# Kernel optimization log

Measured on AMD Instinct MI355X. Metric: run time of the kernel, lower is better.

## Reference

```python
import jax, jax.numpy as jnp
import numpy as np

# Dimensions (match init_kwargs / input_specs)
B, T, D, H, HH, E, L = 256, 512, 256, 256, 128, 32, 2


def setup_inputs() -> dict:
    key = jax.random.key(0)
    ks = jax.random.split(key, 8)
    f32 = jnp.float32
    s_ih = 1.0 / np.sqrt(D)
    s_hh = 1.0 / np.sqrt(H)
    s_hy = 1.0 / np.sqrt(D + H)
    s_hh_hy = 1.0 / np.sqrt(HH)
    s_z = 1.0 / np.sqrt(HH)
    s_d = 1.0 / np.sqrt(E)
    return {
        "input": jax.random.normal(ks[0], (B, T, D), f32),
        # main-cell weights, stacked over layers (layer1 input = hidden = D)
        "Wih": jax.random.normal(ks[1], (L, H, D), f32) * s_ih,
        "Whh": jax.random.normal(ks[2], (L, H, H), f32) * s_hh,
        "b": jnp.zeros((L, H), f32),
        # hyper (meta) RNN cell: input is concat(x_t, h_{t-1})
        "Wih_hy": jax.random.normal(ks[3], (L, HH, D + H), f32) * s_hy,
        "Whh_hy": jax.random.normal(ks[4], (L, HH, HH), f32) * s_hh_hy,
        "b_hy": jnp.zeros((L, HH), f32),
        # embedding projections: hyper_h -> z for (x-scale, h-scale, bias), then z -> d
        "Whz": jax.random.normal(ks[5], (L, 3, E, HH), f32) * s_z,
        "bz": jnp.ones((L, 3, E), f32),  # init z to 1 so d starts near a plain RNN
        "Wzd": jax.random.normal(ks[6], (L, 3, H, E), f32) * s_d,
    }


def reference(input, Wih, Whh, b, Wih_hy, Whh_hy, b_hy, Whz, bz, Wzd):
    """MetaRNN (HyperNetwork-conditioned RNN): for each layer, a small hyper RNN
    consumes [x_t, h_{t-1}] and emits embeddings z that generate per-unit scales
    d_x, d_h and a dynamic bias d_b for the main tanh RNN cell.
    Returns (all hidden states [B,T,H], last hidden state [B,H])."""
    Bb = input.shape[0]
    dt = input.dtype
    x_seq = input
    for l in range(L):
        # input-to-hidden GEMM for the whole sequence, hoisted out of the scan
        xW = jnp.einsum('btd,hd->bth', x_seq, Wih[l])  # [B,T,H]
        Whh_l, b_l = Whh[l], b[l]
        Wih_hy_l, Whh_hy_l, b_hy_l = Wih_hy[l], Whh_hy[l], b_hy[l]
        Whz_l, bz_l, Wzd_l = Whz[l], bz[l], Wzd[l]

        def step(carry, inp):
            h, hh = carry           # main hidden [B,H], hyper hidden [B,HH]
            x_t, xW_t = inp
            hyp_in = jnp.concatenate([x_t, h], axis=1)          # [B, D+H]
            hh_new = jnp.tanh(hyp_in @ Wih_hy_l.T + hh @ Whh_hy_l.T + b_hy_l)
            z = jnp.einsum('bk,gek->bge', hh_new, Whz_l) + bz_l  # [B,3,E]
            d = jnp.einsum('bge,ghe->bgh', z, Wzd_l)             # [B,3,H]
            h_new = jnp.tanh(d[:, 0] * xW_t + d[:, 1] * (h @ Whh_l.T)
                             + d[:, 2] + b_l)
            return (h_new, hh_new), h_new

        h0 = jnp.zeros((Bb, H), dt)
        hh0 = jnp.zeros((Bb, HH), dt)
        xs = (jnp.swapaxes(x_seq, 0, 1), jnp.swapaxes(xW, 0, 1))  # time-major
        _, ys = jax.lax.scan(step, (h0, hh0), xs)
        x_seq = jnp.swapaxes(ys, 0, 1)  # [B,T,H]
    return (x_seq, x_seq[:, -1, :])
```

## Files before the change

### kernel.cpp

```cpp
#include <hip/hip_runtime.h>


#define DEVI __device__ __forceinline__

typedef __bf16 bf16x8 __attribute__((ext_vector_type(8)));
typedef float f32x4 __attribute__((ext_vector_type(4)));
typedef unsigned short u16;
typedef unsigned int u32;
typedef u32 u32x4 __attribute__((ext_vector_type(4)));
typedef u16 u16x8 __attribute__((ext_vector_type(8)));

constexpr int B_ = 256, T_ = 512, D_ = 256, H_ = 256, HH_ = 128, E_ = 32;
constexpr int BT = B_ * T_;

constexpr int OXW = 0,      PXW = 16 * 8 * 512;
constexpr int OXH = 131072, PXH = 8 * 8 * 512;
constexpr int OHY = 196608, PHY = 8 * 12 * 512;
constexpr int OWHH = 294912, PWHH = 16 * 8 * 512;
constexpr int OWHZ = 425984, PWHZ = 6 * 4 * 512;
constexpr int OWZD = 450560, PWZD = 48 * 512;
constexpr int LSTRIDE = 499712;

constexpr size_t WS_XW = 0;
constexpr size_t WS_XH = (size_t)BT * H_ * 4;
constexpr size_t WS_FR = WS_XH + (size_t)BT * HH_ * 4;

DEVI u16 f2bf(float v) {
  u32 u = __float_as_uint(v);
  u += 0x7fffu + ((u >> 16) & 1u);
  return (u16)(u >> 16);
}
DEVI float bf2f(u16 s) { return __uint_as_float(((u32)s) << 16); }
DEVI void split2(float v, u16 &hi, u16 &lo) {
  hi = f2bf(v);
  lo = f2bf(v - bf2f(hi));
}
DEVI bf16x8 ldfrag(const u16 *p) {
  u32x4 v = *reinterpret_cast<const u32x4 *>(p);
  return __builtin_bit_cast(bf16x8, v);
}
DEVI f32x4 mfma3(bf16x8 ah, bf16x8 al, bf16x8 bh, bf16x8 bl, f32x4 c) {
  c = __builtin_amdgcn_mfma_f32_16x16x32_bf16(ah, bh, c, 0, 0, 0);
  c = __builtin_amdgcn_mfma_f32_16x16x32_bf16(ah, bl, c, 0, 0, 0);
  c = __builtin_amdgcn_mfma_f32_16x16x32_bf16(al, bh, c, 0, 0, 0);
  return c;
}
DEVI float tanh_fast(float x) {
  float e = __expf(2.0f * x);
  return 1.0f - 2.0f / (e + 1.0f);
}
DEVI void block_sync() {
  asm volatile("s_waitcnt lgkmcnt(0)\n\ts_barrier" ::: "memory");
}

__global__ void metarnn_prep(const float *__restrict__ Wih,
                             const float *__restrict__ Whh,
                             const float *__restrict__ Wih_hy,
                             const float *__restrict__ Whh_hy,
                             const float *__restrict__ Whz,
                             const float *__restrict__ Wzd,
                             u16 *__restrict__ fr) {
  int gid = blockIdx.x * 256 + threadIdx.x;
  int lane = gid & 63;
  int e = gid >> 6;
  if (e >= 2 * 488) return;
  int l = e / 488, r = e - l * 488;
  u16 *base = fr + (size_t)l * LSTRIDE;
  int rowL = lane & 15, kg = (lane >> 4) << 3;

  const float *src = nullptr;
  int ld = 0, nt = 0, kt = 0, KT = 1, special = 0;
  u16 *dh = nullptr, *dl = nullptr;
  if (r < 128) {
    nt = r >> 3; kt = r & 7; KT = 8;
    src = Wih + (size_t)l * H_ * D_; ld = D_;
    dh = base + OXW; dl = dh + PXW;
  } else if (r < 192) {
    r -= 128; nt = r >> 3; kt = r & 7; KT = 8;
    src = Wih_hy + (size_t)l * HH_ * (D_ + H_); ld = D_ + H_;
    dh = base + OXH; dl = dh + PXH;
  } else if (r < 288) {
    r -= 192; nt = r / 12; kt = r - nt * 12; KT = 12; special = 1;
    dh = base + OHY; dl = dh + PHY;
  } else if (r < 416) {
    r -= 288; nt = r >> 3; kt = r & 7; KT = 8;
    src = Whh + (size_t)l * H_ * H_; ld = H_;
    dh = base + OWHH; dl = dh + PWHH;
  } else if (r < 440) {
    r -= 416; nt = r >> 2; kt = r & 3; KT = 4;
    src = Whz + (size_t)l * 3 * E_ * HH_; ld = HH_;
    dh = base + OWHZ; dl = dh + PWHZ;
  } else {
    r -= 440; int g = r >> 4; nt = r & 15; kt = 0; KT = 1;
    src = Wzd + (size_t)(l * 3 + g) * H_ * E_; ld = E_;
    dh = base + OWZD + g * 16 * 512; dl = base + OWZD + PWZD + g * 16 * 512;
  }
  int row = nt * 16 + rowL;
  long dof = ((long)(nt * KT + kt) * 64 + lane) * 8;
  for (int j = 0; j < 8; ++j) {
    int k = kt * 32 + kg + j;
    float v;
    if (special) {
      v = (k < 256) ? Wih_hy[((size_t)l * HH_ + row) * (D_ + H_) + 256 + k]
                    : Whh_hy[((size_t)l * HH_ + row) * HH_ + (k - 256)];
    } else {
      v = src[(size_t)row * ld + k];
    }
    u16 hi, lo;
    split2(v, hi, lo);
    dh[dof + j] = hi;
    dl[dof + j] = lo;
  }
}

__global__ __launch_bounds__(256, 1) void metarnn_gemm(
    const float *__restrict__ x, const u16 *__restrict__ fr,
    float *__restrict__ xW, float *__restrict__ xH) {
  int w = threadIdx.x >> 6, lane = threadIdx.x & 63;
  int m0 = blockIdx.x * 32;
  int rowL = lane & 15, kg = (lane >> 4) << 3;
  f32x4 acc[2][6] = {};
  const u16 *fxw_h = fr + OXW, *fxw_l = fxw_h + PXW;
  const u16 *fxh_h = fr + OXH, *fxh_l = fxh_h + PXH;

  for (int kt = 0; kt < 8; ++kt) {
    bf16x8 ah[2], al[2];
    for (int s = 0; s < 2; ++s) {
      const float *xp = x + (size_t)(m0 + s * 16 + rowL) * 256 + kt * 32 + kg;
      u16x8 vh, vl;
#pragma unroll
      for (int j = 0; j < 8; ++j) {
        u16 hi, lo;
        split2(xp[j], hi, lo);
        vh[j] = hi; vl[j] = lo;
      }
      ah[s] = __builtin_bit_cast(bf16x8, vh);
      al[s] = __builtin_bit_cast(bf16x8, vl);
    }
#pragma unroll
    for (int q = 0; q < 6; ++q) {
      int nt = w * 6 + q;
      long o = (nt < 16) ? ((long)(nt * 8 + kt) * 64 + lane) * 8
                         : ((long)((nt - 16) * 8 + kt) * 64 + lane) * 8;
      const u16 *bh = (nt < 16) ? fxw_h + o : fxh_h + o;
      const u16 *bl = (nt < 16) ? fxw_l + o : fxh_l + o;
      bf16x8 B0 = ldfrag(bh), B1 = ldfrag(bl);
      acc[0][q] = mfma3(ah[0], al[0], B0, B1, acc[0][q]);
      acc[1][q] = mfma3(ah[1], al[1], B0, B1, acc[1][q]);
    }
  }
  for (int s = 0; s < 2; ++s)
    for (int q = 0; q < 6; ++q) {
      int nt = w * 6 + q;
#pragma unroll
      for (int r = 0; r < 4; ++r) {
        int row = m0 + s * 16 + (lane >> 4) * 4 + r;
        if (nt < 16)
          xW[(size_t)row * H_ + nt * 16 + rowL] = acc[s][q][r];
        else
          xH[(size_t)row * HH_ + (nt - 16) * 16 + rowL] = acc[s][q][r];
      }
    }
}

__global__ __launch_bounds__(512, 2) void metarnn_scan(
    const float *__restrict__ xW, const float *__restrict__ xH,
    const u16 *__restrict__ fr, const float *__restrict__ bmain,
    const float *__restrict__ bhy, const float *__restrict__ bz,
    float *__restrict__ y, float *__restrict__ hlast, int layer, int isLast) {
  __shared__ __align__(16) u16 hc_h[12 * 512];
  __shared__ __align__(16) u16 hc_l[12 * 512];
  __shared__ __align__(16) u16 zf_h[3 * 512];
  __shared__ __align__(16) u16 zf_l[3 * 512];
  __shared__ __align__(16) u16 hy_lds[8 * 12 * 512];

  int tid = threadIdx.x, w = tid >> 6, lane = tid & 63;
  int bs = blockIdx.x * 16;
  int rowL = lane & 15, colG = lane >> 4;

  const u16 *FHY = fr + OHY, *FHYl = FHY + PHY;
  const u16 *FWH = fr + OWHH, *FWHl = FWH + PWHH;
  const u16 *FWZ = fr + OWHZ, *FWZl = FWZ + PWHZ;
  const u16 *FZD = fr + OWZD, *FZDl = FZD + PWZD;

  for (int i = tid; i < 12 * 512; i += 512) { hc_h[i] = 0; hc_l[i] = 0; }
  for (int i = tid; i < 3 * 512; i += 512) { zf_h[i] = 0; zf_l[i] = 0; }
  for (int i = tid; i < 8 * 12 * 512 / 8; i += 512) {
    *reinterpret_cast<u32x4 *>(&hy_lds[(size_t)i * 8]) =
        *reinterpret_cast<const u32x4 *>(FHY + (size_t)i * 8);
  }

  bf16x8 zresH[4], zresL[4];
  {
    int wz = (w < 6) ? w : 0;
#pragma unroll
    for (int kk = 0; kk < 4; ++kk) {
      long o = ((long)(wz * 4 + kk) * 64 + lane) * 8;
      zresH[kk] = ldfrag(FWZ + o);
      zresL[kk] = ldfrag(FWZl + o);
    }
  }
  bf16x8 DH[3][2], DL[3][2];
#pragma unroll
  for (int g = 0; g < 3; ++g)
#pragma unroll
    for (int p = 0; p < 2; ++p) {
      long o = ((long)(g * 16 + 2 * w + p) * 64 + lane) * 8;
      DH[g][p] = ldfrag(FZD + o);
      DL[g][p] = ldfrag(FZDl + o);
    }
  bf16x8 RWL[2][8];
#pragma unroll
  for (int p = 0; p < 2; ++p)
#pragma unroll
    for (int kt = 0; kt < 8; ++kt) {
      long o = ((long)((2 * w + p) * 8 + kt) * 64 + lane) * 8;
      RWL[p][kt] = ldfrag(FWHl + o);
    }

  int c2 = 16 * w + rowL;
  float bhv = bhy[layer * HH_ + c2];
  float bzv = (w < 6) ? bz[layer * 3 * E_ + c2] : 0.0f;
  float bbv[2];
  bbv[0] = bmain[layer * H_ + 32 * w + rowL];
  bbv[1] = bmain[layer * H_ + 32 * w + 16 + rowL];

  bf16x8 bWH[3][2], bYL[3];
#define LOAD_SLOT(S, KT)                                                      \
  {                                                                           \
    long oy = ((long)(w * 12 + (KT)) * 64 + lane) * 8;                        \
    bYL[S] = ldfrag(FHYl + oy);                                               \
    if ((KT) < 8) {                                                           \
      long o0 = ((long)((2 * w) * 8 + (KT)) * 64 + lane) * 8;                 \
      long o1 = ((long)((2 * w + 1) * 8 + (KT)) * 64 + lane) * 8;             \
      bWH[S][0] = ldfrag(FWH + o0);                                           \
      bWH[S][1] = ldfrag(FWH + o1);                                           \
    }                                                                         \
  }
#pragma unroll
  for (int s = 0; s < 3; ++s) LOAD_SLOT(s, s)

  __syncthreads();

  for (int t = 0; t < T_; ++t) {
    float xhv[4], xwv[2][4];
#pragma unroll
    for (int r = 0; r < 4; ++r) {
      size_t row = (size_t)(bs + 4 * colG + r) * T_ + t;
      xhv[r] = xH[row * HH_ + c2];
      xwv[0][r] = xW[row * H_ + 32 * w + rowL];
      xwv[1][r] = xW[row * H_ + 32 * w + 16 + rowL];
    }

    f32x4 aA = {}, aW0 = {}, aW1 = {};
#pragma unroll
    for (int j = 0; j < 12; ++j) {
      const int s = j % 3;
      bf16x8 ah = ldfrag(&hc_h[j * 512 + lane * 8]);
      bf16x8 al = ldfrag(&hc_l[j * 512 + lane * 8]);
      bf16x8 yh = ldfrag(&hy_lds[(w * 12 + j) * 512 + lane * 8]);
      aA = mfma3(ah, al, yh, bYL[s], aA);
      if (j < 8) {
        aW0 = mfma3(ah, al, bWH[s][0], RWL[0][j], aW0);
        aW1 = mfma3(ah, al, bWH[s][1], RWL[1][j], aW1);
      }
      if (j < 9) LOAD_SLOT(s, j + 3)
    }
    block_sync();

#pragma unroll
    for (int s = 0; s < 3; ++s) LOAD_SLOT(s, s)

    {
      int kfr = 8 + (w >> 1);
      int hb2 = 2 * (w & 1) + (rowL >> 3);
      int j7 = rowL & 7;
#pragma unroll
      for (int r = 0; r < 4; ++r) {
        float v = tanh_fast(aA[r] + xhv[r] + bhv);
        u16 hi, lo;
        split2(v, hi, lo);
        int di = kfr * 512 + ((4 * colG + r) + 16 * hb2) * 8 + j7;
        hc_h[di] = hi;
        hc_l[di] = lo;
      }
    }
    block_sync();

    if (w < 6) {
      f32x4 aZ = {};
#pragma unroll
      for (int kk = 0; kk < 4; ++kk) {
        bf16x8 ah = ldfrag(&hc_h[(8 + kk) * 512 + lane * 8]);
        bf16x8 al = ldfrag(&hc_l[(8 + kk) * 512 + lane * 8]);
        aZ = mfma3(ah, al, zresH[kk], zresL[kk], aZ);
      }
      int g = c2 >> 5;
      int hb3 = 2 * (w & 1) + (rowL >> 3);
      int j7 = rowL & 7;
#pragma unroll
      for (int r = 0; r < 4; ++r) {
        float v = aZ[r] + bzv;
        u16 hi, lo;
        split2(v, hi, lo);
        int di = g * 512 + ((4 * colG + r) + 16 * hb3) * 8 + j7;
        zf_h[di] = hi;
        zf_l[di] = lo;
      }
    }
    block_sync();

    float arg[2][4];
#pragma unroll
    for (int p = 0; p < 2; ++p)
#pragma unroll
      for (int r = 0; r < 4; ++r) arg[p][r] = bbv[p];
#pragma unroll
    for (int g = 0; g < 3; ++g) {
      bf16x8 zh = ldfrag(&zf_h[g * 512 + lane * 8]);
      bf16x8 zl = ldfrag(&zf_l[g * 512 + lane * 8]);
#pragma unroll
      for (int p = 0; p < 2; ++p) {
        f32x4 zero = {};
        f32x4 dg = mfma3(zh, zl, DH[g][p], DL[g][p], zero);
#pragma unroll
        for (int r = 0; r < 4; ++r) {
          float mul = (g == 0) ? xwv[p][r]
                    : (g == 1) ? ((p == 0) ? aW0[r] : aW1[r]) : 1.0f;
          arg[p][r] += dg[r] * mul;
        }
      }
    }
#pragma unroll
    for (int p = 0; p < 2; ++p) {
      int c = 32 * w + 16 * p + rowL;
      int hb6 = 2 * p + (rowL >> 3);
      int j7 = rowL & 7;
#pragma unroll
      for (int r = 0; r < 4; ++r) {
        int m = 4 * colG + r;
        float h = tanh_fast(arg[p][r]);
        size_t gi = (size_t)(bs + m) * T_ + t;
        y[gi * H_ + c] = h;
        if (isLast && t == T_ - 1) hlast[(size_t)(bs + m) * H_ + c] = h;
        u16 hi, lo;
        split2(h, hi, lo);
        int di = w * 512 + (m + 16 * hb6) * 8 + j7;
        hc_h[di] = hi;
        hc_l[di] = lo;
      }
    }
    block_sync();
  }
#undef LOAD_SLOT
}

extern "C" void kernel_launch(void *const *d_in, const int *in_sizes, int n_in,
                              void *d_out, int out_size, void *d_ws,
                              size_t ws_size, hipStream_t stream) {
  (void)in_sizes; (void)n_in; (void)out_size; (void)ws_size;
  const float *input  = (const float *)d_in[0];
  const float *Wih    = (const float *)d_in[1];
  const float *Whh    = (const float *)d_in[2];
  const float *b      = (const float *)d_in[3];
  const float *Wih_hy = (const float *)d_in[4];
  const float *Whh_hy = (const float *)d_in[5];
  const float *b_hy   = (const float *)d_in[6];
  const float *Whz    = (const float *)d_in[7];
  const float *bz     = (const float *)d_in[8];
  const float *Wzd    = (const float *)d_in[9];

  float *out = (float *)d_out;
  float *xW = (float *)((char *)d_ws + WS_XW);
  float *xH = (float *)((char *)d_ws + WS_XH);
  u16 *fr = (u16 *)((char *)d_ws + WS_FR);
  float *hlast = out + (size_t)BT * H_;

  metarnn_prep<<<dim3(244), dim3(256), 0, stream>>>(Wih, Whh, Wih_hy, Whh_hy,
                                                    Whz, Wzd, fr);
  for (int l = 0; l < 2; ++l) {
    const float *xsrc = (l == 0) ? input : out;
    const u16 *frl = fr + (size_t)l * LSTRIDE;
    metarnn_gemm<<<dim3(BT / 32), dim3(256), 0, stream>>>(xsrc, frl, xW, xH);
    metarnn_scan<<<dim3(16), dim3(512), 0, stream>>>(
        xW, xH, frl, b, b_hy, bz, out, hlast, l, (l == 1) ? 1 : 0);
  }
}
```

Baseline: 9.033 ms.

## Double-buffer hyper hidden state to drop a per-step barrier, split accumulators

Moves the hyper hidden state into a ping-pong LDS buffer indexed by timestep parity. This lets the barrier after the recurrent MFMA loop be removed, since new hyper values no longer overwrite fragments other waves are still reading. It also splits the hyper accumulator into even/odd chains to shorten MFMA dependency chains, raises wave priority during the MFMA loop, and pins register-resident weights with empty asm so they are not rematerialized. The cost is extra LDS and a correctness dependence on the remaining barriers ordering the main-h writes.

```diff
diff --git a/kernel.cpp b/kernel.cpp
--- a/kernel.cpp
+++ b/kernel.cpp
@@ -38,6 +38,11 @@
 DEVI bf16x8 ldfrag(const u16 *p) {
   u32x4 v = *reinterpret_cast<const u32x4 *>(p);
   return __builtin_bit_cast(bf16x8, v);
+}
+DEVI void pin(bf16x8 &x) {
+  u32x4 t = __builtin_bit_cast(u32x4, x);
+  asm volatile("" : "+v"(t));
+  x = __builtin_bit_cast(bf16x8, t);
 }
 DEVI f32x4 mfma3(bf16x8 ah, bf16x8 al, bf16x8 bh, bf16x8 bl, f32x4 c) {
   c = __builtin_amdgcn_mfma_f32_16x16x32_bf16(ah, bh, c, 0, 0, 0);
@@ -168,8 +173,10 @@
     const u16 *__restrict__ fr, const float *__restrict__ bmain,
     const float *__restrict__ bhy, const float *__restrict__ bz,
     float *__restrict__ y, float *__restrict__ hlast, int layer, int isLast) {
-  __shared__ __align__(16) u16 hc_h[12 * 512];
-  __shared__ __align__(16) u16 hc_l[12 * 512];
+  __shared__ __align__(16) u16 hc_h[8 * 512];
+  __shared__ __align__(16) u16 hc_l[8 * 512];
+  __shared__ __align__(16) u16 hhb_h[2][4 * 512];
+  __shared__ __align__(16) u16 hhb_l[2][4 * 512];
   __shared__ __align__(16) u16 zf_h[3 * 512];
   __shared__ __align__(16) u16 zf_l[3 * 512];
   __shared__ __align__(16) u16 hy_lds[8 * 12 * 512];
@@ -183,7 +190,10 @@
   const u16 *FWZ = fr + OWHZ, *FWZl = FWZ + PWHZ;
   const u16 *FZD = fr + OWZD, *FZDl = FZD + PWZD;
 
-  for (int i = tid; i < 12 * 512; i += 512) { hc_h[i] = 0; hc_l[i] = 0; }
+  for (int i = tid; i < 8 * 512; i += 512) { hc_h[i] = 0; hc_l[i] = 0; }
+  for (int i = tid; i < 4 * 512; i += 512) {
+    hhb_h[0][i] = 0; hhb_l[0][i] = 0; hhb_h[1][i] = 0; hhb_l[1][i] = 0;
+  }
   for (int i = tid; i < 3 * 512; i += 512) { zf_h[i] = 0; zf_l[i] = 0; }
   for (int i = tid; i < 8 * 12 * 512 / 8; i += 512) {
     *reinterpret_cast<u32x4 *>(&hy_lds[(size_t)i * 8]) =
@@ -196,8 +206,8 @@
 #pragma unroll
     for (int kk = 0; kk < 4; ++kk) {
       long o = ((long)(wz * 4 + kk) * 64 + lane) * 8;
-      zresH[kk] = ldfrag(FWZ + o);
-      zresL[kk] = ldfrag(FWZl + o);
+      zresH[kk] = ldfrag(FWZ + o);  pin(zresH[kk]);
+      zresL[kk] = ldfrag(FWZl + o); pin(zresL[kk]);
     }
   }
   bf16x8 DH[3][2], DL[3][2];
@@ -206,8 +216,8 @@
 #pragma unroll
     for (int p = 0; p < 2; ++p) {
       long o = ((long)(g * 16 + 2 * w + p) * 64 + lane) * 8;
-      DH[g][p] = ldfrag(FZD + o);
-      DL[g][p] = ldfrag(FZDl + o);
+      DH[g][p] = ldfrag(FZD + o);  pin(DH[g][p]);
+      DL[g][p] = ldfrag(FZDl + o); pin(DL[g][p]);
     }
   bf16x8 RWL[2][8];
 #pragma unroll
@@ -216,6 +226,7 @@
     for (int kt = 0; kt < 8; ++kt) {
       long o = ((long)((2 * w + p) * 8 + kt) * 64 + lane) * 8;
       RWL[p][kt] = ldfrag(FWHl + o);
+      pin(RWL[p][kt]);
     }
 
   int c2 = 16 * w + rowL;
@@ -243,6 +254,7 @@
   __syncthreads();
 
   for (int t = 0; t < T_; ++t) {
+    const int pr = t & 1;
     float xhv[4], xwv[2][4];
 #pragma unroll
     for (int r = 0; r < 4; ++r) {
@@ -252,27 +264,38 @@
       xwv[1][r] = xW[row * H_ + 32 * w + 16 + rowL];
     }
 
-    f32x4 aA = {}, aW0 = {}, aW1 = {};
+    f32x4 aAe = {}, aAo = {}, aW0 = {}, aW1 = {};
+    __builtin_amdgcn_s_setprio(1);
 #pragma unroll
     for (int j = 0; j < 12; ++j) {
       const int s = j % 3;
-      bf16x8 ah = ldfrag(&hc_h[j * 512 + lane * 8]);
-      bf16x8 al = ldfrag(&hc_l[j * 512 + lane * 8]);
+      bf16x8 ah, al;
+      if (j < 8) {
+        ah = ldfrag(&hc_h[j * 512 + lane * 8]);
+        al = ldfrag(&hc_l[j * 512 + lane * 8]);
+      } else {
+        ah = ldfrag(&hhb_h[pr ^ 1][(j - 8) * 512 + lane * 8]);
+        al = ldfrag(&hhb_l[pr ^ 1][(j - 8) * 512 + lane * 8]);
+      }
       bf16x8 yh = ldfrag(&hy_lds[(w * 12 + j) * 512 + lane * 8]);
-      aA = mfma3(ah, al, yh, bYL[s], aA);
+      if (j & 1) aAo = mfma3(ah, al, yh, bYL[s], aAo);
+      else       aAe = mfma3(ah, al, yh, bYL[s], aAe);
       if (j < 8) {
         aW0 = mfma3(ah, al, bWH[s][0], RWL[0][j], aW0);
         aW1 = mfma3(ah, al, bWH[s][1], RWL[1][j], aW1);
       }
       if (j < 9) LOAD_SLOT(s, j + 3)
     }
-    block_sync();
+    __builtin_amdgcn_s_setprio(0);
+    f32x4 aA;
+#pragma unroll
+    for (int r = 0; r < 4; ++r) aA[r] = aAe[r] + aAo[r];
 
 #pragma unroll
     for (int s = 0; s < 3; ++s) LOAD_SLOT(s, s)
 
     {
-      int kfr = 8 + (w >> 1);
+      int kfr = w >> 1;
       int hb2 = 2 * (w & 1) + (rowL >> 3);
       int j7 = rowL & 7;
 #pragma unroll
@@ -281,8 +304,8 @@
         u16 hi, lo;
         split2(v, hi, lo);
         int di = kfr * 512 + ((4 * colG + r) + 16 * hb2) * 8 + j7;
-        hc_h[di] = hi;
-        hc_l[di] = lo;
+        hhb_h[pr][di] = hi;
+        hhb_l[pr][di] = lo;
       }
     }
     block_sync();
@@ -291,8 +314,8 @@
       f32x4 aZ = {};
 #pragma unroll
       for (int kk = 0; kk < 4; ++kk) {
-        bf16x8 ah = ldfrag(&hc_h[(8 + kk) * 512 + lane * 8]);
-        bf16x8 al = ldfrag(&hc_l[(8 + kk) * 512 + lane * 8]);
+        bf16x8 ah = ldfrag(&hhb_h[pr][kk * 512 + lane * 8]);
+        bf16x8 al = ldfrag(&hhb_l[pr][kk * 512 + lane * 8]);
         aZ = mfma3(ah, al, zresH[kk], zresL[kk], aZ);
       }
       int g = c2 >> 5;
@@ -345,7 +368,7 @@
         if (isLast && t == T_ - 1) hlast[(size_t)(bs + m) * H_ + c] = h;
         u16 hi, lo;
         split2(h, hi, lo);
-        int di = w * 512 + (m + 16 * hb6) * 8 + j7;
+        int di = (c >> 5) * 512 + (m + 16 * hb6) * 8 + j7;
         hc_h[di] = hi;
         hc_l[di] = lo;
       }
```

Result: faster. 8.796 ms (-2.6%).
